# Kernel tuning notes

Hardware: AMD Instinct MI355X
Metric: run time of the kernel (lower is better)

Reference implementation:

```python
import jax, jax.numpy as jnp
import numpy as np

N_NODES = 100000
N_EDGES = 1600000
D_IN = 128
D_OUT = 128
K_HOPS = 2


def gcn_norm(edge_index, num_nodes):
    # Add self-loops (weight 1), compute symmetric normalization
    # norm_e = deg^{-1/2}[src] * deg^{-1/2}[dst], deg over destination index.
    loop = jnp.arange(num_nodes, dtype=edge_index.dtype)
    src = jnp.concatenate([edge_index[0], loop])
    dst = jnp.concatenate([edge_index[1], loop])
    w = jnp.ones(src.shape[0], dtype=jnp.float32)
    deg = jax.ops.segment_sum(w, dst, num_segments=num_nodes)
    dinv = jnp.where(deg > 0, jax.lax.rsqrt(deg), 0.0)
    norm = dinv[src] * dinv[dst]
    return src, dst, norm


def setup_inputs() -> dict:
    key = jax.random.key(0)
    k1, k2, k3, k4 = jax.random.split(key, 4)
    x = jax.random.normal(k1, (N_NODES, D_IN), dtype=jnp.float32)
    edge_index = jax.random.randint(k2, (2, N_EDGES), 0, N_NODES, dtype=jnp.int64)
    # SGConv linear params (Glorot-ish scale)
    W = jax.random.normal(k3, (D_IN, D_OUT), dtype=jnp.float32) / np.sqrt(D_IN)
    b = jnp.zeros((D_OUT,), dtype=jnp.float32)
    return {"x": x, "edge_index": edge_index, "W": W, "b": b}


def reference(x, edge_index, W, b):
    n = x.shape[0]
    src, dst, norm = gcn_norm(edge_index, n)
    h = x
    for _ in range(K_HOPS):
        # gather source features, scale by edge norm, scatter-add to destinations
        h = jax.ops.segment_sum(h[src] * norm[:, None], dst, num_segments=n)
    return h @ W + b
```

## Files before the change

kernel.cpp:

```cpp
#include <hip/hip_runtime.h>
#include <hip/hip_bf16.h>


#define DFEAT 128
#define ELLW 64
#define ABLK 2048
#define CAP 4608
#define NBUCKMAX 512

typedef __attribute__((ext_vector_type(8))) short short8;
typedef __attribute__((ext_vector_type(4))) float f32x4;
typedef __attribute__((ext_vector_type(4))) unsigned int u32x4;
typedef __attribute__((ext_vector_type(4))) int i32x4;

__device__ __forceinline__ float bf2f(unsigned short u) {
    union { unsigned int i; float f; } t;
    t.i = ((unsigned int)u) << 16;
    return t.f;
}

__device__ __forceinline__ unsigned short f2bf(float f) {
    union { float f; unsigned int i; } t;
    t.f = f;
    unsigned int lsb = (t.i >> 16) & 1u;
    t.i += 0x7fffu + lsb;
    return (unsigned short)(t.i >> 16);
}

__device__ __forceinline__ void accum8(float* acc, uint4 u, float w) {
    acc[0] += bf2f((unsigned short)(u.x & 0xffffu)) * w;
    acc[1] += bf2f((unsigned short)(u.x >> 16)) * w;
    acc[2] += bf2f((unsigned short)(u.y & 0xffffu)) * w;
    acc[3] += bf2f((unsigned short)(u.y >> 16)) * w;
    acc[4] += bf2f((unsigned short)(u.z & 0xffffu)) * w;
    acc[5] += bf2f((unsigned short)(u.z >> 16)) * w;
    acc[6] += bf2f((unsigned short)(u.w & 0xffffu)) * w;
    acc[7] += bf2f((unsigned short)(u.w >> 16)) * w;
}

__device__ __forceinline__ void add8(float* acc, uint4 u) {
    union { unsigned int i; float f; } a;
    a.i = u.x << 16;          acc[0] += a.f;
    a.i = u.x & 0xffff0000u;  acc[1] += a.f;
    a.i = u.y << 16;          acc[2] += a.f;
    a.i = u.y & 0xffff0000u;  acc[3] += a.f;
    a.i = u.z << 16;          acc[4] += a.f;
    a.i = u.z & 0xffff0000u;  acc[5] += a.f;
    a.i = u.w << 16;          acc[6] += a.f;
    a.i = u.w & 0xffff0000u;  acc[7] += a.f;
}

__global__ void k_detect(const unsigned short* __restrict__ xs,
                         const int* __restrict__ ei, int* __restrict__ flags) {
    int t = blockIdx.x * 256 + (int)threadIdx.x;
    int bad = 0;
    for (int i = t; i < 16384; i += 2048) {
        unsigned int e = (xs[i] >> 7) & 0xFFu;
        if (e >= 0xC0u) bad = 1;
    }
    if (__any(bad) && (threadIdx.x & 63) == 0) atomicOr(flags, 1);
    int oddnz = 0;
    for (int i = t; i < 4096; i += 2048) {
        if (ei[2 * i + 1] != 0) oddnz = 1;
    }
    if (__any(oddnz) && (threadIdx.x & 63) == 0) atomicOr(flags + 1, 1);
}

__global__ void k_prepB(const void* __restrict__ Wraw, const int* __restrict__ flags,
                        unsigned short* __restrict__ Bf) {
    int t = blockIdx.x * 256 + threadIdx.x;
    if (t >= 2048) return;
    int lane = t & 63;
    int chunk = (t >> 6) & 3;
    int ntile = t >> 8;
    int ncol = ntile * 16 + (lane & 15);
    int k0 = chunk * 32 + (lane >> 4) * 8;
    int isf = flags[0];
    const float* Wf = (const float*)Wraw;
    const unsigned short* Wb = (const unsigned short*)Wraw;
    unsigned short* o = Bf + (size_t)t * 8;
#pragma unroll
    for (int j = 0; j < 8; j++) {
        int idx = (k0 + j) * DFEAT + ncol;
        o[j] = isf ? f2bf(Wf[idx]) : Wb[idx];
    }
}

__global__ __launch_bounds__(256) void k_bucketA(const int* __restrict__ ei, int E, int n,
                                                 const int* __restrict__ flags,
                                                 int* __restrict__ bucketCnt,
                                                 unsigned int* __restrict__ buck) {
    __shared__ int sdst[ABLK];
    __shared__ int ssrc[ABLK];
    __shared__ int hist[NBUCKMAX];
    __shared__ int base_[NBUCKMAX];
    int tid = (int)threadIdx.x;
    for (int t = tid; t < NBUCKMAX; t += 256) hist[t] = 0;
    __syncthreads();
    int e0 = blockIdx.x * ABLK;
    int i64 = (flags[1] == 0);

    if (e0 + ABLK <= E) {
        int d[8], s[8];
#pragma unroll
        for (int k = 0; k < 8; k++) {
            int e = e0 + tid + k * 256;
            d[k] = i64 ? __builtin_nontemporal_load(ei + 2 * (E + e))
                       : __builtin_nontemporal_load(ei + E + e);
        }
#pragma unroll
        for (int k = 0; k < 8; k++) {
            int e = e0 + tid + k * 256;
            s[k] = i64 ? __builtin_nontemporal_load(ei + 2 * e)
                       : __builtin_nontemporal_load(ei + e);
        }
#pragma unroll
        for (int k = 0; k < 8; k++) {
            sdst[tid + k * 256] = d[k];
            ssrc[tid + k * 256] = s[k];
            atomicAdd(&hist[d[k] >> 8], 1);
        }
    } else {
        for (int e = e0 + tid; e < E; e += 256) {
            int d = i64 ? ei[2 * (E + e)] : ei[E + e];
            int s = i64 ? ei[2 * e] : ei[e];
            sdst[e - e0] = d;
            ssrc[e - e0] = s;
            atomicAdd(&hist[d >> 8], 1);
        }
    }
    __syncthreads();
#pragma unroll
    for (int r = 0; r < 2; r++) {
        int t = (tid + r * 256 + (int)blockIdx.x * 61) & (NBUCKMAX - 1);
        int cc = hist[t];
        base_[t] = cc ? atomicAdd(bucketCnt + t, cc) : 0;
        hist[t] = 0;
    }
    __syncthreads();
    int nloc = min(ABLK, E - e0);
    if (nloc == ABLK) {
#pragma unroll
        for (int k = 0; k < 8; k++) {
            int idx = tid + k * 256;
            int d = sdst[idx], s = ssrc[idx];
            int b = d >> 8;
            int pos = base_[b] + atomicAdd(&hist[b], 1);
            if (pos < CAP)
                buck[(size_t)b * CAP + pos] =
                    (unsigned int)s | ((unsigned int)(d & 255) << 17);
        }
    } else {
        for (int idx = tid; idx < nloc; idx += 256) {
            int d = sdst[idx], s = ssrc[idx];
            int b = d >> 8;
            int pos = base_[b] + atomicAdd(&hist[b], 1);
            if (pos < CAP)
                buck[(size_t)b * CAP + pos] =
                    (unsigned int)s | ((unsigned int)(d & 255) << 17);
        }
    }
}

__global__ __launch_bounds__(256) void k_bucketB_gemm0(
        const unsigned int* __restrict__ buck,
        const int* __restrict__ bucketCnt, int n,
        int* __restrict__ cnt, int* __restrict__ ell,
        const void* __restrict__ xraw,
        const unsigned short* __restrict__ Bf,
        const int* __restrict__ flags,
        unsigned short* __restrict__ g0) {
    __shared__ int lcnt[256];
    __shared__ unsigned short thi[16 * 136];
    __shared__ unsigned short tlo[16 * 136];
    int b = blockIdx.x;
    int tid = (int)threadIdx.x;
    lcnt[tid] = 0;
    __syncthreads();

    int m0 = min(bucketCnt[b], CAP);
    int node0 = b << 8;
    const unsigned int* bp = buck + (size_t)b * CAP;
    for (int base = 0; base < m0; base += 1024) {
        unsigned int w[4];
#pragma unroll
        for (int j = 0; j < 4; j++) {
            int i = base + tid + j * 256;
            w[j] = (i < m0) ? __builtin_nontemporal_load(bp + i) : 0xFFFFFFFFu;
        }
#pragma unroll
        for (int j = 0; j < 4; j++) {
            if (w[j] != 0xFFFFFFFFu) {
                int s = (int)(w[j] & 0x1FFFFu);
                int dl = (int)(w[j] >> 17);
                int pos = atomicAdd(&lcnt[dl], 1);
                if (pos < ELLW) ell[(size_t)(node0 + dl) * ELLW + pos] = s;
            }
        }
    }
    __syncthreads();
    {
        int node = node0 + tid;
        if (node < n) {
            int c = lcnt[tid];
            cnt[node] = c;
            int st = min(c, ELLW);
            int slots = min((c + 16) & ~15, ELLW);
            int* rowp = ell + (size_t)node * ELLW;
            for (int p = st; p < slots; p++) rowp[p] = node;
        }
    }

    int isf = flags[0];
    int wave = tid >> 6;
    int lane = tid & 63;
    int g = lane >> 4, c = lane & 15;
    int trow = wave * 4 + g;

    for (int tile = 0; tile < 16; ++tile) {
        int lrow = tile * 16 + trow;
        int node = node0 + lrow;
        uint4 ohi = {0, 0, 0, 0}, olo = {0, 0, 0, 0};
        if (node < n) {
            if (isf) {
                const float* xf = (const float*)xraw;
                f32x4 v0 = __builtin_nontemporal_load((const f32x4*)(xf + (size_t)node * DFEAT + c * 8));
                f32x4 v1 = __builtin_nontemporal_load((const f32x4*)(xf + (size_t)node * DFEAT + c * 8 + 4));
                float vv[8] = {v0[0], v0[1], v0[2], v0[3], v1[0], v1[1], v1[2], v1[3]};
                unsigned short h[8], l[8];
#pragma unroll
                for (int j = 0; j < 8; j++) {
                    h[j] = f2bf(vv[j]);
                    l[j] = f2bf(vv[j] - bf2f(h[j]));
                }
                ohi.x = (unsigned int)h[0] | ((unsigned int)h[1] << 16);
                ohi.y = (unsigned int)h[2] | ((unsigned int)h[3] << 16);
                ohi.z = (unsigned int)h[4] | ((unsigned int)h[5] << 16);
                ohi.w = (unsigned int)h[6] | ((unsigned int)h[7] << 16);
                olo.x = (unsigned int)l[0] | ((unsigned int)l[1] << 16);
                olo.y = (unsigned int)l[2] | ((unsigned int)l[3] << 16);
                olo.z = (unsigned int)l[4] | ((unsigned int)l[5] << 16);
                olo.w = (unsigned int)l[6] | ((unsigned int)l[7] << 16);
            } else {
                u32x4 u = __builtin_nontemporal_load(
                    (const u32x4*)((const unsigned short*)xraw + (size_t)node * DFEAT + c * 8));
                ohi.x = u[0]; ohi.y = u[1]; ohi.z = u[2]; ohi.w = u[3];
            }
        }
        __syncthreads();
        *(uint4*)(thi + trow * 136 + c * 8) = ohi;
        *(uint4*)(tlo + trow * 136 + c * 8) = olo;
        __syncthreads();

        int m = c, quad = g;
        f32x4 acc2[2];
        acc2[0] = (f32x4){0.f, 0.f, 0.f, 0.f};
        acc2[1] = (f32x4){0.f, 0.f, 0.f, 0.f};
#pragma unroll
        for (int c2 = 0; c2 < 4; c2++) {
            short8 ah = *(const short8*)(thi + m * 136 + c2 * 32 + quad * 8);
            short8 al = *(const short8*)(tlo + m * 136 + c2 * 32 + quad * 8);
#pragma unroll
            for (int t = 0; t < 2; t++) {
                int nt = wave * 2 + t;
                short8 bfr = *(const short8*)(Bf + ((size_t)(nt * 4 + c2) * 64 + lane) * 8);
                acc2[t] = __builtin_amdgcn_mfma_f32_16x16x32_bf16(ah, bfr, acc2[t], 0, 0, 0);
                acc2[t] = __builtin_amdgcn_mfma_f32_16x16x32_bf16(al, bfr, acc2[t], 0, 0, 0);
            }
        }

        float sc[4];
#pragma unroll
        for (int r2 = 0; r2 < 4; r2++) {
            int lr = tile * 16 + quad * 4 + r2;
            sc[r2] = (node0 + lr < n) ? rsqrtf((float)(lcnt[lr] + 1)) : 0.f;
        }
#pragma unroll
        for (int t = 0; t < 2; t++) {
            int col = (wave * 2 + t) * 16 + m;
#pragma unroll
            for (int r2 = 0; r2 < 4; r2++) {
                int gnode = node0 + tile * 16 + quad * 4 + r2;
                if (gnode < n)
                    g0[(size_t)gnode * DFEAT + col] = f2bf(acc2[t][r2] * sc[r2]);
            }
        }
    }
}

__device__ __forceinline__ void hop_accum(const unsigned short* __restrict__ fb,
                                          const int* __restrict__ ell,
                                          int node, int cn, int lane, float* acc) {
    int g = lane >> 4, c = lane & 15;
    int slots = min((cn + 16) & ~15, ELLW);
    const int* row = ell + (size_t)node * ELLW;
#pragma unroll
    for (int j = 0; j < 8; j++) acc[j] = 0.f;

    for (int base = 0; base < slots; base += 16) {
        i32x4 s4 = __builtin_nontemporal_load((const i32x4*)(row + base) + g);
        uint4 u0 = *(const uint4*)(fb + (size_t)s4[0] * DFEAT + c * 8);
        uint4 u1 = *(const uint4*)(fb + (size_t)s4[1] * DFEAT + c * 8);
        uint4 u2 = *(const uint4*)(fb + (size_t)s4[2] * DFEAT + c * 8);
        uint4 u3 = *(const uint4*)(fb + (size_t)s4[3] * DFEAT + c * 8);
        add8(acc, u0);
        add8(acc, u1);
        add8(acc, u2);
        add8(acc, u3);
    }
    float corrw = (cn < ELLW) ? (float)(cn + 1 - slots) : 1.0f;
    if (g == 0 && corrw != 0.0f) {
        uint4 u = *(const uint4*)(fb + (size_t)node * DFEAT + c * 8);
        accum8(acc, u, corrw);
    }
#pragma unroll
    for (int j = 0; j < 8; j++) {
        acc[j] += __shfl_xor(acc[j], 16);
        acc[j] += __shfl_xor(acc[j], 32);
    }
}

__global__ __launch_bounds__(256) void k_hop(const unsigned short* __restrict__ src,
                                             const int* __restrict__ ell,
                                             const int* __restrict__ cnt,
                                             unsigned short* __restrict__ outb, int n) {
    int node = blockIdx.x * 4 + (threadIdx.x >> 6);
    if (node >= n) return;
    int lane = threadIdx.x & 63;
    int cn = cnt[node];
    float acc[8];
    hop_accum(src, ell, node, cn, lane, acc);
    if ((lane >> 4) == 0) {
        int c = lane & 15;
        float sc = 1.0f / (float)(cn + 1);
        uint4 o;
        o.x = (unsigned int)f2bf(acc[0] * sc) | ((unsigned int)f2bf(acc[1] * sc) << 16);
        o.y = (unsigned int)f2bf(acc[2] * sc) | ((unsigned int)f2bf(acc[3] * sc) << 16);
        o.z = (unsigned int)f2bf(acc[4] * sc) | ((unsigned int)f2bf(acc[5] * sc) << 16);
        o.w = (unsigned int)f2bf(acc[6] * sc) | ((unsigned int)f2bf(acc[7] * sc) << 16);
        *(uint4*)(outb + (size_t)node * DFEAT + c * 8) = o;
    }
}

__global__ __launch_bounds__(256) void k_hop2_out(const unsigned short* __restrict__ src,
                                                  const int* __restrict__ ell,
                                                  const int* __restrict__ cnt,
                                                  const void* __restrict__ braw,
                                                  const int* __restrict__ flags,
                                                  void* __restrict__ outraw, int n) {
    int node = blockIdx.x * 4 + (threadIdx.x >> 6);
    if (node >= n) return;
    int lane = threadIdx.x & 63;
    int cn = cnt[node];
    float acc[8];
    hop_accum(src, ell, node, cn, lane, acc);
    if ((lane >> 4) == 0) {
        int c = lane & 15;
        float sc = rsqrtf((float)(cn + 1));
        int isf = flags[0];
        const float* bf32 = (const float*)braw;
        const unsigned short* bb16 = (const unsigned short*)braw;
#pragma unroll
        for (int j = 0; j < 8; j++) {
            float bias = isf ? bf32[c * 8 + j] : bf2f(bb16[c * 8 + j]);
            acc[j] = acc[j] * sc + bias;
        }
        if (isf) {
            float* outf = (float*)outraw;
            *(float4*)(outf + (size_t)node * DFEAT + c * 8) =
                (float4){acc[0], acc[1], acc[2], acc[3]};
            *(float4*)(outf + (size_t)node * DFEAT + c * 8 + 4) =
                (float4){acc[4], acc[5], acc[6], acc[7]};
        } else {
            unsigned short* outb = (unsigned short*)outraw;
            uint4 o;
            o.x = (unsigned int)f2bf(acc[0]) | ((unsigned int)f2bf(acc[1]) << 16);
            o.y = (unsigned int)f2bf(acc[2]) | ((unsigned int)f2bf(acc[3]) << 16);
            o.z = (unsigned int)f2bf(acc[4]) | ((unsigned int)f2bf(acc[5]) << 16);
            o.w = (unsigned int)f2bf(acc[6]) | ((unsigned int)f2bf(acc[7]) << 16);
            *(uint4*)(outb + (size_t)node * DFEAT + c * 8) = o;
        }
    }
}

extern "C" void kernel_launch(void* const* d_in, const int* in_sizes, int n_in,
                              void* d_out, int out_size, void* d_ws, size_t ws_size,
                              hipStream_t stream) {
    const void* x = d_in[0];
    const int* ei = (const int*)d_in[1];
    const void* W = d_in[2];
    const void* b = d_in[3];

    const int n = in_sizes[0] / DFEAT;
    const int E = in_sizes[1] / 2;

    int* ell = (int*)d_ws;
    unsigned short* g1 = (unsigned short*)(ell + (size_t)n * ELLW);
    int* cnt = (int*)(g1 + (size_t)n * DFEAT);
    int* flags = cnt + n;
    int* bucketCnt = flags + 4;
    unsigned short* Bf = (unsigned short*)(bucketCnt + NBUCKMAX);
    unsigned short* g0 = (unsigned short*)d_out;
    unsigned int* buck = (unsigned int*)g1;

    (void)hipMemsetAsync(flags, 0, (4 + NBUCKMAX) * sizeof(int), stream);

    k_detect<<<8, 256, 0, stream>>>((const unsigned short*)x, ei, flags);

    k_prepB<<<8, 256, 0, stream>>>(W, flags, Bf);

    int nbuck = (n + 255) >> 8;
    int ablocks = (E + ABLK - 1) / ABLK;
    k_bucketA<<<ablocks, 256, 0, stream>>>(ei, E, n, flags, bucketCnt, buck);

    k_bucketB_gemm0<<<nbuck, 256, 0, stream>>>(buck, bucketCnt, n, cnt, ell,
                                               x, Bf, flags, g0);

    k_hop<<<(n + 3) / 4, 256, 0, stream>>>(g0, ell, cnt, g1, n);

    k_hop2_out<<<(n + 3) / 4, 256, 0, stream>>>(g1, ell, cnt, b, flags, d_out, n);
}
```

Baseline: 308.1 us.

## Fuse setup kernels, split bucket blocks, pad ELL to 8, split hop launches

Merges the flag detection, weight prep and memset into one setup kernel that also zeroes the bucket counters, removing a memset and a launch. The bucket/GEMM kernel now runs two blocks per 256-node bucket, each handling 128 nodes, which doubles parallelism but makes each block re-read the whole bucket list. ELL rows are padded to multiples of 8 instead of 16, with a half-group tail step in the gather to avoid loading dummy self-neighbours. The hop kernels are each launched twice over node halves, which adds launches without an obvious locality benefit.

```diff
diff --git a/kernel.cpp b/kernel.cpp
--- a/kernel.cpp
+++ b/kernel.cpp
@@ -50,34 +50,42 @@
     a.i = u.w & 0xffff0000u;  acc[7] += a.f;
 }
 
-__global__ void k_detect(const unsigned short* __restrict__ xs,
-                         const int* __restrict__ ei, int* __restrict__ flags) {
-    int t = blockIdx.x * 256 + (int)threadIdx.x;
+__global__ __launch_bounds__(256) void k_setup(const unsigned short* __restrict__ xs,
+                                               const int* __restrict__ ei,
+                                               const void* __restrict__ Wraw,
+                                               int* __restrict__ flags,
+                                               int* __restrict__ bucketCnt,
+                                               unsigned short* __restrict__ Bf) {
+    __shared__ int s_f32, s_odd;
+    int tid = (int)threadIdx.x;
+    if (tid == 0) { s_f32 = 0; s_odd = 0; }
+    __syncthreads();
     int bad = 0;
-    for (int i = t; i < 16384; i += 2048) {
+    for (int i = tid; i < 16384; i += 256) {
         unsigned int e = (xs[i] >> 7) & 0xFFu;
         if (e >= 0xC0u) bad = 1;
     }
-    if (__any(bad) && (threadIdx.x & 63) == 0) atomicOr(flags, 1);
-    int oddnz = 0;
-    for (int i = t; i < 4096; i += 2048) {
-        if (ei[2 * i + 1] != 0) oddnz = 1;
-    }
-    if (__any(oddnz) && (threadIdx.x & 63) == 0) atomicOr(flags + 1, 1);
-}
-
-__global__ void k_prepB(const void* __restrict__ Wraw, const int* __restrict__ flags,
-                        unsigned short* __restrict__ Bf) {
-    int t = blockIdx.x * 256 + threadIdx.x;
-    if (t >= 2048) return;
+    if (bad) atomicOr(&s_f32, 1);
+    int odd = 0;
+    for (int i = tid; i < 4096; i += 256) {
+        if (ei[2 * i + 1] != 0) odd = 1;
+    }
+    if (odd) atomicOr(&s_odd, 1);
+    if (blockIdx.x == 0) {
+        for (int i = tid; i < NBUCKMAX; i += 256) bucketCnt[i] = 0;
+    }
+    __syncthreads();
+    int isf = s_f32;
+    if (blockIdx.x == 0 && tid == 0) { flags[0] = s_f32; flags[1] = s_odd; }
+
+    const float* Wf = (const float*)Wraw;
+    const unsigned short* Wb = (const unsigned short*)Wraw;
+    int t = (int)blockIdx.x * 256 + tid;
     int lane = t & 63;
     int chunk = (t >> 6) & 3;
     int ntile = t >> 8;
     int ncol = ntile * 16 + (lane & 15);
     int k0 = chunk * 32 + (lane >> 4) * 8;
-    int isf = flags[0];
-    const float* Wf = (const float*)Wraw;
-    const unsigned short* Wb = (const unsigned short*)Wraw;
     unsigned short* o = Bf + (size_t)t * 8;
 #pragma unroll
     for (int j = 0; j < 8; j++) {
@@ -170,16 +178,17 @@
         const unsigned short* __restrict__ Bf,
         const int* __restrict__ flags,
         unsigned short* __restrict__ g0) {
-    __shared__ int lcnt[256];
+    __shared__ int lcnt[128];
     __shared__ unsigned short thi[16 * 136];
     __shared__ unsigned short tlo[16 * 136];
-    int b = blockIdx.x;
+    int b = blockIdx.x >> 1;
+    int h = blockIdx.x & 1;
     int tid = (int)threadIdx.x;
-    lcnt[tid] = 0;
+    if (tid < 128) lcnt[tid] = 0;
     __syncthreads();
 
     int m0 = min(bucketCnt[b], CAP);
-    int node0 = b << 8;
+    int node0 = (b << 8) + (h << 7);
     const unsigned int* bp = buck + (size_t)b * CAP;
     for (int base = 0; base < m0; base += 1024) {
         unsigned int w[4];
@@ -191,21 +200,24 @@
 #pragma unroll
         for (int j = 0; j < 4; j++) {
             if (w[j] != 0xFFFFFFFFu) {
-                int s = (int)(w[j] & 0x1FFFFu);
                 int dl = (int)(w[j] >> 17);
-                int pos = atomicAdd(&lcnt[dl], 1);
-                if (pos < ELLW) ell[(size_t)(node0 + dl) * ELLW + pos] = s;
+                if ((dl >> 7) == h) {
+                    int s = (int)(w[j] & 0x1FFFFu);
+                    int pos = atomicAdd(&lcnt[dl & 127], 1);
+                    if (pos < ELLW)
+                        ell[(size_t)((b << 8) + dl) * ELLW + pos] = s;
+                }
             }
         }
     }
     __syncthreads();
-    {
+    if (tid < 128) {
         int node = node0 + tid;
         if (node < n) {
             int c = lcnt[tid];
             cnt[node] = c;
             int st = min(c, ELLW);
-            int slots = min((c + 16) & ~15, ELLW);
+            int slots = min((c + 8) & ~7, ELLW);
             int* rowp = ell + (size_t)node * ELLW;
             for (int p = st; p < slots; p++) rowp[p] = node;
         }
@@ -217,7 +229,7 @@
     int g = lane >> 4, c = lane & 15;
     int trow = wave * 4 + g;
 
-    for (int tile = 0; tile < 16; ++tile) {
+    for (int tile = 0; tile < 8; ++tile) {
         int lrow = tile * 16 + trow;
         int node = node0 + lrow;
         uint4 ohi = {0, 0, 0, 0}, olo = {0, 0, 0, 0};
@@ -227,20 +239,20 @@
                 f32x4 v0 = __builtin_nontemporal_load((const f32x4*)(xf + (size_t)node * DFEAT + c * 8));
                 f32x4 v1 = __builtin_nontemporal_load((const f32x4*)(xf + (size_t)node * DFEAT + c * 8 + 4));
                 float vv[8] = {v0[0], v0[1], v0[2], v0[3], v1[0], v1[1], v1[2], v1[3]};
-                unsigned short h[8], l[8];
+                unsigned short hh[8], ll[8];
 #pragma unroll
                 for (int j = 0; j < 8; j++) {
-                    h[j] = f2bf(vv[j]);
-                    l[j] = f2bf(vv[j] - bf2f(h[j]));
+                    hh[j] = f2bf(vv[j]);
+                    ll[j] = f2bf(vv[j] - bf2f(hh[j]));
                 }
-                ohi.x = (unsigned int)h[0] | ((unsigned int)h[1] << 16);
-                ohi.y = (unsigned int)h[2] | ((unsigned int)h[3] << 16);
-                ohi.z = (unsigned int)h[4] | ((unsigned int)h[5] << 16);
-                ohi.w = (unsigned int)h[6] | ((unsigned int)h[7] << 16);
-                olo.x = (unsigned int)l[0] | ((unsigned int)l[1] << 16);
-                olo.y = (unsigned int)l[2] | ((unsigned int)l[3] << 16);
-                olo.z = (unsigned int)l[4] | ((unsigned int)l[5] << 16);
-                olo.w = (unsigned int)l[6] | ((unsigned int)l[7] << 16);
+                ohi.x = (unsigned int)hh[0] | ((unsigned int)hh[1] << 16);
+                ohi.y = (unsigned int)hh[2] | ((unsigned int)hh[3] << 16);
+                ohi.z = (unsigned int)hh[4] | ((unsigned int)hh[5] << 16);
+                ohi.w = (unsigned int)hh[6] | ((unsigned int)hh[7] << 16);
+                olo.x = (unsigned int)ll[0] | ((unsigned int)ll[1] << 16);
+                olo.y = (unsigned int)ll[2] | ((unsigned int)ll[3] << 16);
+                olo.z = (unsigned int)ll[4] | ((unsigned int)ll[5] << 16);
+                olo.w = (unsigned int)ll[6] | ((unsigned int)ll[7] << 16);
             } else {
                 u32x4 u = __builtin_nontemporal_load(
                     (const u32x4*)((const unsigned short*)xraw + (size_t)node * DFEAT + c * 8));
@@ -292,12 +304,13 @@
                                           const int* __restrict__ ell,
                                           int node, int cn, int lane, float* acc) {
     int g = lane >> 4, c = lane & 15;
-    int slots = min((cn + 16) & ~15, ELLW);
+    int slots = min((cn + 8) & ~7, ELLW);
+    int full = slots & ~15;
     const int* row = ell + (size_t)node * ELLW;
 #pragma unroll
     for (int j = 0; j < 8; j++) acc[j] = 0.f;
 
-    for (int base = 0; base < slots; base += 16) {
+    for (int base = 0; base < full; base += 16) {
         i32x4 s4 = __builtin_nontemporal_load((const i32x4*)(row + base) + g);
         uint4 u0 = *(const uint4*)(fb + (size_t)s4[0] * DFEAT + c * 8);
         uint4 u1 = *(const uint4*)(fb + (size_t)s4[1] * DFEAT + c * 8);
@@ -308,6 +321,17 @@
         add8(acc, u2);
         add8(acc, u3);
     }
+    if (full < slots && g < 2) {
+        i32x4 s4 = __builtin_nontemporal_load((const i32x4*)(row + full) + g);
+        uint4 u0 = *(const uint4*)(fb + (size_t)s4[0] * DFEAT + c * 8);
+        uint4 u1 = *(const uint4*)(fb + (size_t)s4[1] * DFEAT + c * 8);
+        uint4 u2 = *(const uint4*)(fb + (size_t)s4[2] * DFEAT + c * 8);
+        uint4 u3 = *(const uint4*)(fb + (size_t)s4[3] * DFEAT + c * 8);
+        add8(acc, u0);
+        add8(acc, u1);
+        add8(acc, u2);
+        add8(acc, u3);
+    }
     float corrw = (cn < ELLW) ? (float)(cn + 1 - slots) : 1.0f;
     if (g == 0 && corrw != 0.0f) {
         uint4 u = *(const uint4*)(fb + (size_t)node * DFEAT + c * 8);
@@ -323,9 +347,10 @@
 __global__ __launch_bounds__(256) void k_hop(const unsigned short* __restrict__ src,
                                              const int* __restrict__ ell,
                                              const int* __restrict__ cnt,
-                                             unsigned short* __restrict__ outb, int n) {
-    int node = blockIdx.x * 4 + (threadIdx.x >> 6);
-    if (node >= n) return;
+                                             unsigned short* __restrict__ outb,
+                                             int n0, int n1) {
+    int node = n0 + blockIdx.x * 4 + (threadIdx.x >> 6);
+    if (node >= n1) return;
     int lane = threadIdx.x & 63;
     int cn = cnt[node];
     float acc[8];
@@ -347,9 +372,10 @@
                                                   const int* __restrict__ cnt,
                                                   const void* __restrict__ braw,
                                                   const int* __restrict__ flags,
-                                                  void* __restrict__ outraw, int n) {
-    int node = blockIdx.x * 4 + (threadIdx.x >> 6);
-    if (node >= n) return;
+                                                  void* __restrict__ outraw,
+                                                  int n0, int n1) {
+    int node = n0 + blockIdx.x * 4 + (threadIdx.x >> 6);
+    if (node >= n1) return;
     int lane = threadIdx.x & 63;
     int cn = cnt[node];
     float acc[8];
@@ -403,20 +429,20 @@
     unsigned short* g0 = (unsigned short*)d_out;
     unsigned int* buck = (unsigned int*)g1;
 
-    (void)hipMemsetAsync(flags, 0, (4 + NBUCKMAX) * sizeof(int), stream);
-
-    k_detect<<<8, 256, 0, stream>>>((const unsigned short*)x, ei, flags);
-
-    k_prepB<<<8, 256, 0, stream>>>(W, flags, Bf);
+    k_setup<<<8, 256, 0, stream>>>((const unsigned short*)x, ei, W,
+                                   flags, bucketCnt, Bf);
 
     int nbuck = (n + 255) >> 8;
     int ablocks = (E + ABLK - 1) / ABLK;
     k_bucketA<<<ablocks, 256, 0, stream>>>(ei, E, n, flags, bucketCnt, buck);
 
-    k_bucketB_gemm0<<<nbuck, 256, 0, stream>>>(buck, bucketCnt, n, cnt, ell,
-                                               x, Bf, flags, g0);
-
-    k_hop<<<(n + 3) / 4, 256, 0, stream>>>(g0, ell, cnt, g1, n);
-
-    k_hop2_out<<<(n + 3) / 4, 256, 0, stream>>>(g1, ell, cnt, b, flags, d_out, n);
-}
+    k_bucketB_gemm0<<<2 * nbuck, 256, 0, stream>>>(buck, bucketCnt, n, cnt, ell,
+                                                   x, Bf, flags, g0);
+
+    int half = ((n / 2) + 3) & ~3;
+    k_hop<<<(half + 3) / 4, 256, 0, stream>>>(g0, ell, cnt, g1, 0, half);
+    k_hop<<<((n - half) + 3) / 4, 256, 0, stream>>>(g0, ell, cnt, g1, half, n);
+
+    k_hop2_out<<<(half + 3) / 4, 256, 0, stream>>>(g1, ell, cnt, b, flags, d_out, 0, half);
+    k_hop2_out<<<((n - half) + 3) / 4, 256, 0, stream>>>(g1, ell, cnt, b, flags, d_out, half, n);
+}
```

New measurement: 329.4 us. 6.9% more time.
